# Optimization experiments

Hardware: AMD Instinct MI355X
Metric: run time of the kernel (lower is better)

Reference implementation:

```python
import jax, jax.numpy as jnp
import numpy as np

D_MODEL = 512
NHEAD = 8
HEAD_DIM = D_MODEL // NHEAD  # 64
BUCKETS = 32                 # lsh_hash_bucket_size; hashes >= 32 never attended (faithful to source loop)
N_HASHES = 2
B, T = 2, 2048


def setup_inputs() -> dict:
    key = jax.random.key(0)
    ks = jax.random.split(key, 14)
    s = 1.0 / np.sqrt(D_MODEL)
    sh = 1.0 / np.sqrt(HEAD_DIM)
    return {
        "query": jax.random.normal(ks[0], (B, T, D_MODEL), dtype=jnp.float32),
        "key": jax.random.normal(ks[1], (B, T, D_MODEL), dtype=jnp.float32),
        "value": jax.random.normal(ks[2], (B, T, D_MODEL), dtype=jnp.float32),
        "Wq": jax.random.normal(ks[3], (D_MODEL, D_MODEL), dtype=jnp.float32) * s,
        "bq": jnp.zeros((D_MODEL,), jnp.float32),
        "Wk": jax.random.normal(ks[4], (D_MODEL, D_MODEL), dtype=jnp.float32) * s,
        "bk": jnp.zeros((D_MODEL,), jnp.float32),
        "Wv": jax.random.normal(ks[5], (D_MODEL, D_MODEL), dtype=jnp.float32) * s,
        "bv": jnp.zeros((D_MODEL,), jnp.float32),
        "Wo": jax.random.normal(ks[6], (D_MODEL, D_MODEL), dtype=jnp.float32) * s,
        "bo": jnp.zeros((D_MODEL,), jnp.float32),
        "lsh_W": jax.random.normal(ks[7], (N_HASHES, HEAD_DIM, HEAD_DIM), dtype=jnp.float32) * sh,
        "lsh_b": jax.random.normal(ks[8], (N_HASHES, HEAD_DIM), dtype=jnp.float32) * sh,
    }


def reference(query, key, value, Wq, bq, Wk, bk, Wv, bv, Wo, bo, lsh_W, lsh_b):
    B0, Nt, E = query.shape
    H, Dh = NHEAD, E // NHEAD

    def lin(x, W, b):  # torch nn.Linear: x @ W.T + b
        return x @ W.T + b

    # Source transposes (0,1) then reshape(B0, Nt, H, Dh); reshape on the
    # contiguous transposed tensor == jnp reshape of swapaxes result.
    q = lin(jnp.swapaxes(query, 0, 1), Wq, bq).reshape(B0, Nt, H, Dh).transpose(0, 2, 1, 3)
    k = lin(jnp.swapaxes(key, 0, 1), Wk, bk).reshape(B0, Nt, H, Dh).transpose(0, 2, 1, 3)
    v = lin(jnp.swapaxes(value, 0, 1), Wv, bv).reshape(B0, Nt, H, Dh).transpose(0, 2, 1, 3)

    scale = 1.0 / jnp.sqrt(jnp.asarray(Dh, q.dtype))
    neg = jnp.finfo(q.dtype).min
    acc = jnp.zeros_like(q)
    for i in range(N_HASHES):
        # argmax(softmax(x)) == argmax(x)
        qh = jnp.argmax(q @ lsh_W[i].T + lsh_b[i], axis=-1)  # [B,H,T]
        kh = jnp.argmax(k @ lsh_W[i].T + lsh_b[i], axis=-1)  # [B,H,T]
        # attend only within same bucket AND bucket id < BUCKETS (source loops 0..BUCKETS-1)
        mask = (qh[..., :, None] == kh[..., None, :]) & (qh[..., :, None] < BUCKETS)
        scores = jnp.einsum('bhtd,bhsd->bhts', q, k) * scale
        probs = jax.nn.softmax(jnp.where(mask, scores, neg), axis=-1)
        valid = mask.any(axis=-1)  # queries with >=1 key in-bucket; others stay zero
        out_i = jnp.einsum('bhts,bhsd->bhtd', probs, v)
        acc = acc + jnp.where(valid[..., None], out_i, jnp.zeros((), q.dtype))
    out = acc / N_HASHES  # mean over hash rounds

    out = out.transpose(0, 2, 1, 3).reshape(B0, Nt, E)
    out = lin(out, Wo, bo)
    return jnp.swapaxes(out, 0, 1)  # [Nt, B0, E]
```

## Files before the change

kernel.cpp:

```cpp
#include <hip/hip_runtime.h>
#include <stdint.h>
#include <math.h>


#define T_ 2048
#define E_ 512
#define H_ 8
#define DH_ 64
#define B_ 2
#define M_ 4096
#define NROUND 2
#define NBUCKET 32
#define NSEG 32
#define MAXTASK 5120

typedef short v8s __attribute__((ext_vector_type(8)));
typedef _Float16 v8h __attribute__((ext_vector_type(8)));
typedef float v4f __attribute__((ext_vector_type(4)));

__device__ __forceinline__ float bf2f(uint16_t u) {
  union { uint32_t i; float f; } v; v.i = ((uint32_t)u) << 16; return v.f;
}
__device__ __forceinline__ uint16_t f2bf(float f) {
  union { float fv; uint32_t i; } v; v.fv = f;
  uint32_t x = v.i;
  x += 0x7fffu + ((x >> 16) & 1u);
  return (uint16_t)(x >> 16);
}
__device__ __forceinline__ void split8(const float4 a, const float4 b,
                                       v8s& h, v8s& l) {
  const float x[8] = {a.x, a.y, a.z, a.w, b.x, b.y, b.z, b.w};
#pragma unroll
  for (int j = 0; j < 8; j++) {
    const uint16_t hh = f2bf(x[j]);
    h[j] = (short)hh;
    l[j] = (short)f2bf(x[j] - bf2f(hh));
  }
}
__device__ __forceinline__ void split2h8(const float4 a, const float4 b,
                                         v8h& h, v8h& l) {
  const float x[8] = {a.x, a.y, a.z, a.w, b.x, b.y, b.z, b.w};
#pragma unroll
  for (int j = 0; j < 8; j++) {
    const float xv = x[j];
    const _Float16 hh = (fabsf(xv) < 6.1035156e-5f) ? (_Float16)0.0f
                                                    : (_Float16)xv;
    const float r = xv - (float)hh;
    h[j] = hh;
    l[j] = (_Float16)(r * 4096.0f);
  }
}

__global__ __launch_bounds__(256) void prep_kernel(
    const float* __restrict__ Xq, const float* __restrict__ Xk,
    const float* __restrict__ Xv,
    const float* __restrict__ Wq, const float* __restrict__ Wk,
    const float* __restrict__ Wv, const float* __restrict__ Wo,
    const float* __restrict__ lshW,
    uint16_t* __restrict__ Xqh, uint16_t* __restrict__ Xql,
    uint16_t* __restrict__ Xkh, uint16_t* __restrict__ Xkl,
    uint16_t* __restrict__ Xvh, uint16_t* __restrict__ Xvl,
    uint16_t* __restrict__ Wqh, uint16_t* __restrict__ Wql,
    uint16_t* __restrict__ Wkh, uint16_t* __restrict__ Wkl,
    uint16_t* __restrict__ Wvh, uint16_t* __restrict__ Wvl,
    uint16_t* __restrict__ Woh, uint16_t* __restrict__ Wol,
    uint16_t* __restrict__ Lwh, uint16_t* __restrict__ Lwl,
    float* __restrict__ attn, int* __restrict__ cnt)
{
  const int bid = blockIdx.x;
  const int tid = threadIdx.x;

  if (bid < 384) {
    const int sel = bid >> 7;
    const int mb  = bid & 127;
    const float* X = (sel == 0) ? Xq : (sel == 1) ? Xk : Xv;
    uint16_t* H = (sel == 0) ? Xqh : (sel == 1) ? Xkh : Xvh;
    uint16_t* L = (sel == 0) ? Xql : (sel == 1) ? Xkl : Xvl;
#pragma unroll
    for (int it = 0; it < 8; it++) {
      const int g = it * 256 + tid;
      const int f = g >> 6;
      const int lane = g & 63;
      const int ks = f >> 1, half = f & 1;
      const int p = mb * 32 + half * 16 + (lane & 15);
      const int k = ks * 32 + (lane >> 4) * 8;
      const long src = ((long)(p & 1) * T_ + (p >> 1)) * E_ + k;
      const float4 a = *(const float4*)(X + src);
      const float4 b = *(const float4*)(X + src + 4);
      v8h h, l;
      split2h8(a, b, h, l);
      const long dst = (long)mb * 16384 + (long)g * 8;
      *(v8h*)(H + dst) = h;
      *(v8h*)(L + dst) = l;
    }
    return;
  }

  if (bid < 896) {
    const int wsel = (bid - 384) >> 7;
    const int g2 = ((bid - 384) & 127) * 256 + tid;
    const int f = g2 >> 6;
    const int lane = g2 & 63;
    const int nb = f >> 4, ks = f & 15;
    const int n = nb * 16 + (lane & 15);
    const int k = ks * 32 + (lane >> 4) * 8;
    const long src = (long)n * E_ + k;
    const long dst = (long)g2 * 8;
    if (wsel < 3) {
      const float* S = (wsel == 0) ? Wq : (wsel == 1) ? Wk : Wv;
      const float4 a = *(const float4*)(S + src);
      const float4 b = *(const float4*)(S + src + 4);
      v8h h, l;
      split2h8(a, b, h, l);
      uint16_t* H = (wsel == 0) ? Wqh : (wsel == 1) ? Wkh : Wvh;
      uint16_t* L = (wsel == 0) ? Wql : (wsel == 1) ? Wkl : Wvl;
      *(v8h*)(H + dst) = h;
      *(v8h*)(L + dst) = l;
    } else {
      const float4 a = *(const float4*)(Wo + src);
      const float4 b = *(const float4*)(Wo + src + 4);
      v8s h, l;
      split8(a, b, h, l);
      *(v8s*)(Woh + dst) = h;
      *(v8s*)(Wol + dst) = l;
    }
    return;
  }

  if (bid < 1920) {
    float4* a4 = (float4*)attn;
    const int g = (bid - 896) * 512 + tid * 2;
    a4[g] = make_float4(0.f, 0.f, 0.f, 0.f);
    a4[g + 1] = make_float4(0.f, 0.f, 0.f, 0.f);
    return;
  }

  for (int i = tid; i < 2 * NSEG * NBUCKET + 1; i += 256) cnt[i] = 0;
  for (int i = tid; i < NROUND * DH_ * DH_; i += 256) {
    const float xv = lshW[i];
    const _Float16 hh = (fabsf(xv) < 6.1035156e-5f) ? (_Float16)0.0f
                                                    : (_Float16)xv;
    const float r = xv - (float)hh;
    *(_Float16*)(Lwh + i) = hh;
    *(_Float16*)(Lwl + i) = (_Float16)(r * 4096.0f);
  }
}

__global__ __launch_bounds__(256) void proj_mfma(
    const uint16_t* __restrict__ Aqh, const uint16_t* __restrict__ Aql,
    const uint16_t* __restrict__ Akh, const uint16_t* __restrict__ Akl,
    const uint16_t* __restrict__ Avh, const uint16_t* __restrict__ Avl,
    const uint16_t* __restrict__ Bqh, const uint16_t* __restrict__ Bql,
    const uint16_t* __restrict__ Bkh, const uint16_t* __restrict__ Bkl,
    const uint16_t* __restrict__ Bvh, const uint16_t* __restrict__ Bvl,
    const float* __restrict__ bq, const float* __restrict__ bk,
    const float* __restrict__ bv,
    float* __restrict__ Qo, float* __restrict__ Ko, float* __restrict__ Vo)
{
  const uint16_t *Ah, *Al, *Bh, *Bl;
  const float* bias; float* C;
  if (blockIdx.z == 0)      { Ah = Aqh; Al = Aql; Bh = Bqh; Bl = Bql; bias = bq; C = Qo; }
  else if (blockIdx.z == 1) { Ah = Akh; Al = Akl; Bh = Bkh; Bl = Bkl; bias = bk; C = Ko; }
  else                      { Ah = Avh; Al = Avl; Bh = Bvh; Bl = Bvl; bias = bv; C = Vo; }

  const int wid = threadIdx.x >> 6, lane = threadIdx.x & 63;
  const int mb = blockIdx.x * 4 + wid;
  const int nb0 = blockIdx.y * 4;
  const int m0 = mb * 32, n0 = blockIdx.y * 64;
  const int l15 = lane & 15, quad = lane >> 4;

  const long aB = (long)mb * 16384 + lane * 8;
  long bB[4];
#pragma unroll
  for (int j = 0; j < 4; j++) bB[j] = (long)(nb0 + j) * 8192 + lane * 8;

  v4f accH[2][4] = {};
  v4f accX[2][4] = {};

  v8h ah0 = *(const v8h*)(Ah + aB);
  v8h ah1 = *(const v8h*)(Ah + aB + 512);
  v8h al0 = *(const v8h*)(Al + aB);
  v8h al1 = *(const v8h*)(Al + aB + 512);
  v8h bh[4], bl[4];
#pragma unroll
  for (int j = 0; j < 4; j++) {
    bh[j] = *(const v8h*)(Bh + bB[j]);
    bl[j] = *(const v8h*)(Bl + bB[j]);
  }

  for (int ks = 0; ks < 16; ks++) {
    const int kn = (ks + 1) & 15;
    const v8h nah0 = *(const v8h*)(Ah + aB + kn * 1024);
    const v8h nah1 = *(const v8h*)(Ah + aB + kn * 1024 + 512);
    const v8h nal0 = *(const v8h*)(Al + aB + kn * 1024);
    const v8h nal1 = *(const v8h*)(Al + aB + kn * 1024 + 512);
    v8h nbh[4], nbl[4];
#pragma unroll
    for (int j = 0; j < 4; j++) {
      nbh[j] = *(const v8h*)(Bh + bB[j] + kn * 512);
      nbl[j] = *(const v8h*)(Bl + bB[j] + kn * 512);
    }

#pragma unroll
    for (int j = 0; j < 4; j++) {
      accH[0][j] = __builtin_amdgcn_mfma_f32_16x16x32_f16(ah0, bh[j], accH[0][j], 0, 0, 0);
      accH[1][j] = __builtin_amdgcn_mfma_f32_16x16x32_f16(ah1, bh[j], accH[1][j], 0, 0, 0);
    }
#pragma unroll
    for (int j = 0; j < 4; j++) {
      accX[0][j] = __builtin_amdgcn_mfma_f32_16x16x32_f16(ah0, bl[j], accX[0][j], 0, 0, 0);
      accX[1][j] = __builtin_amdgcn_mfma_f32_16x16x32_f16(ah1, bl[j], accX[1][j], 0, 0, 0);
    }
#pragma unroll
    for (int j = 0; j < 4; j++) {
      accX[0][j] = __builtin_amdgcn_mfma_f32_16x16x32_f16(al0, bh[j], accX[0][j], 0, 0, 0);
      accX[1][j] = __builtin_amdgcn_mfma_f32_16x16x32_f16(al1, bh[j], accX[1][j], 0, 0, 0);
    }

    ah0 = nah0; al0 = nal0; ah1 = nah1; al1 = nal1;
#pragma unroll
    for (int j = 0; j < 4; j++) { bh[j] = nbh[j]; bl[j] = nbl[j]; }
  }

#pragma unroll
  for (int i = 0; i < 2; i++)
#pragma unroll
    for (int j = 0; j < 4; j++) {
      const int colg = n0 + j * 16 + l15;
      const float bb = bias[colg];
#pragma unroll
      for (int r = 0; r < 4; r++) {
        const int mm = m0 + i * 16 + quad * 4 + r;
        C[(long)mm * E_ + colg] =
            accH[i][j][r] + accX[i][j][r] * (1.0f / 4096.0f) + bb;
      }
    }
}

__global__ __launch_bounds__(256) void mfma_gemm(
    const float* __restrict__ A,
    const uint16_t* __restrict__ Bht, const uint16_t* __restrict__ Blt,
    const float* __restrict__ bias, float* __restrict__ C)
{
  const int wid = threadIdx.x >> 6, lane = threadIdx.x & 63;
  const int mb = blockIdx.x * 4 + wid;
  const int m0 = mb * 32;
  const int nb0 = blockIdx.y * 4;
  const int n0 = blockIdx.y * 64;
  const int l15 = lane & 15, quad = lane >> 4;

  const long aB = (long)mb * 16384 + lane * 8;
  long bB[4];
#pragma unroll
  for (int j = 0; j < 4; j++) bB[j] = (long)(nb0 + j) * 8192 + lane * 8;

  v4f acc[2][4] = {};
  for (int ks = 0; ks < 16; ks++) {
    const long a0 = aB + ks * 1024;
    const long a1 = a0 + 512;
    v8s ah0, al0, ah1, al1;
    split8(*(const float4*)(A + a0), *(const float4*)(A + a0 + 4), ah0, al0);
    split8(*(const float4*)(A + a1), *(const float4*)(A + a1 + 4), ah1, al1);
    v8s bh[4], bl[4];
#pragma unroll
    for (int j = 0; j < 4; j++) {
      bh[j] = *(const v8s*)(Bht + bB[j] + ks * 512);
      bl[j] = *(const v8s*)(Blt + bB[j] + ks * 512);
    }
#pragma unroll
    for (int j = 0; j < 4; j++) {
      acc[0][j] = __builtin_amdgcn_mfma_f32_16x16x32_bf16(ah0, bh[j], acc[0][j], 0, 0, 0);
      acc[1][j] = __builtin_amdgcn_mfma_f32_16x16x32_bf16(ah1, bh[j], acc[1][j], 0, 0, 0);
    }
#pragma unroll
    for (int j = 0; j < 4; j++) {
      acc[0][j] = __builtin_amdgcn_mfma_f32_16x16x32_bf16(ah0, bl[j], acc[0][j], 0, 0, 0);
      acc[1][j] = __builtin_amdgcn_mfma_f32_16x16x32_bf16(ah1, bl[j], acc[1][j], 0, 0, 0);
    }
#pragma unroll
    for (int j = 0; j < 4; j++) {
      acc[0][j] = __builtin_amdgcn_mfma_f32_16x16x32_bf16(al0, bh[j], acc[0][j], 0, 0, 0);
      acc[1][j] = __builtin_amdgcn_mfma_f32_16x16x32_bf16(al1, bh[j], acc[1][j], 0, 0, 0);
    }
  }

#pragma unroll
  for (int i = 0; i < 2; i++)
#pragma unroll
    for (int j = 0; j < 4; j++) {
      const int colg = n0 + j * 16 + l15;
      const float bb = bias[colg];
#pragma unroll
      for (int r = 0; r < 4; r++) {
        const int mm = m0 + i * 16 + quad * 4 + r;
        const int crow = (mm & (T_ - 1)) * B_ + (mm >> 11);
        C[(long)crow * E_ + colg] = acc[i][j][r] + bb;
      }
    }
}

__global__ __launch_bounds__(256) void hash_mfma(
    const float* __restrict__ Q, const float* __restrict__ K,
    const uint16_t* __restrict__ Lwh, const uint16_t* __restrict__ Lwl,
    const float* __restrict__ lshb,
    int* __restrict__ qh, int* __restrict__ kh,
    int* __restrict__ qcnt, int* __restrict__ kcnt)
{
  const int comb = blockIdx.y;
  const int src = comb >> 1, r = comb & 1;
  const float* X = src ? K : Q;
  int* outh = src ? kh : qh;
  int* cnt  = src ? kcnt : qcnt;

  const int wid = threadIdx.x >> 6, lane = threadIdx.x & 63;
  const int m0 = (blockIdx.x * 4 + wid) * 32;
  const int l15 = lane & 15, quad = lane >> 4;

  v8h bh[4][2], bl[4][2];
#pragma unroll
  for (int n = 0; n < 4; n++)
#pragma unroll
    for (int k = 0; k < 2; k++) {
      const int o = r * (DH_ * DH_) + (n * 16 + l15) * DH_ + k * 32 + quad * 8;
      bh[n][k] = *(const v8h*)(Lwh + o);
      bl[n][k] = *(const v8h*)(Lwl + o);
    }

  v4f accH[2][4] = {};
  v4f accX[2][4] = {};
#pragma unroll
  for (int k = 0; k < 2; k++) {
    const long a0 = (long)(m0 + l15) * DH_ + k * 32 + quad * 8;
    const long a1 = a0 + 16L * DH_;
    v8h ah0, al0, ah1, al1;
    split2h8(*(const float4*)(X + a0), *(const float4*)(X + a0 + 4), ah0, al0);
    split2h8(*(const float4*)(X + a1), *(const float4*)(X + a1 + 4), ah1, al1);
#pragma unroll
    for (int n = 0; n < 4; n++) {
      accH[0][n] = __builtin_amdgcn_mfma_f32_16x16x32_f16(ah0, bh[n][k], accH[0][n], 0, 0, 0);
      accH[1][n] = __builtin_amdgcn_mfma_f32_16x16x32_f16(ah1, bh[n][k], accH[1][n], 0, 0, 0);
      accX[0][n] = __builtin_amdgcn_mfma_f32_16x16x32_f16(ah0, bl[n][k], accX[0][n], 0, 0, 0);
      accX[1][n] = __builtin_amdgcn_mfma_f32_16x16x32_f16(ah1, bl[n][k], accX[1][n], 0, 0, 0);
      accX[0][n] = __builtin_amdgcn_mfma_f32_16x16x32_f16(al0, bh[n][k], accX[0][n], 0, 0, 0);
      accX[1][n] = __builtin_amdgcn_mfma_f32_16x16x32_f16(al1, bh[n][k], accX[1][n], 0, 0, 0);
    }
  }

  float bb[4];
#pragma unroll
  for (int n = 0; n < 4; n++) bb[n] = lshb[r * DH_ + n * 16 + l15];

#pragma unroll
  for (int i = 0; i < 2; i++)
#pragma unroll
    for (int reg = 0; reg < 4; reg++) {
      float bv = -INFINITY; int bi = 0x7fffffff;
#pragma unroll
      for (int n = 0; n < 4; n++) {
        const float v = accH[i][n][reg] + accX[i][n][reg] * (1.0f / 4096.0f)
                        + bb[n];
        const int idx = n * 16 + l15;
        if (v > bv || (v == bv && idx < bi)) { bv = v; bi = idx; }
      }
#pragma unroll
      for (int d = 8; d >= 1; d >>= 1) {
        const float ov = __shfl_xor(bv, d);
        const int oi = __shfl_xor(bi, d);
        if (ov > bv || (ov == bv && oi < bi)) { bv = ov; bi = oi; }
      }
      if (l15 == 0) {
        const int hr = m0 + i * 16 + quad * 4 + reg;
        const int p = hr >> 3, hh = hr & 7;
        const int bt = p >> 11, t = p & (T_ - 1);
        const int seg = r * 16 + bt * H_ + hh;
        outh[seg * T_ + t] = bi;
        if (bi < NBUCKET) atomicAdd(&cnt[seg * NBUCKET + bi], 1);
      }
    }
}

__global__ __launch_bounds__(1024) void scan_kernel(
    const int* __restrict__ kcnt, int* __restrict__ koff,
    int* __restrict__ kcur,
    const int* __restrict__ qcnt, int* __restrict__ qoff,
    int* __restrict__ qcur,
    int* __restrict__ ntasks, int* __restrict__ tasks)
{
  const int tid = threadIdx.x;
  const int isq = blockIdx.x;
  const int seg = tid >> 5;
  const int b   = tid & 31;
  const int* cnt = isq ? qcnt : kcnt;
  int* off = isq ? qoff : koff;
  int* cur = isq ? qcur : kcur;

  const int c = cnt[seg * NBUCKET + b];

  int s = c;
#pragma unroll
  for (int d = 1; d < 32; d <<= 1) {
    const int t = __shfl_up(s, d, 32);
    if (b >= d) s += t;
  }
  const int excl = s - c;
  off[seg * (NBUCKET + 1) + b] = excl;
  cur[seg * NBUCKET + b] = excl;
  if (b == 31) off[seg * (NBUCKET + 1) + NBUCKET] = s;

  if (isq) {
    const int nt = (c + 15) >> 4;
    const int lane = tid & 63;
    int ws = nt;
#pragma unroll
    for (int d = 1; d < 64; d <<= 1) {
      const int t = __shfl_up(ws, d, 64);
      if (lane >= d) ws += t;
    }
    const int wtotal = __shfl(ws, 63, 64);
    int base = 0;
    if (lane == 63 && wtotal > 0) base = atomicAdd(ntasks, wtotal);
    base = __shfl(base, 63, 64);
    const int my = base + ws - nt;
    for (int i = 0; i < nt; i++)
      tasks[my + i] = (seg << 16) | (b << 8) | i;
  }
}

__global__ __launch_bounds__(256) void scatter2_kernel(
    const int* __restrict__ kh, const int* __restrict__ qh,
    int* __restrict__ kcur, int* __restrict__ qcur,
    int* __restrict__ klist, int* __restrict__ qlist)
{
  const int idx = blockIdx.x * 256 + threadIdx.x;
  const int y = blockIdx.y;
  const int* hsh = y ? qh : kh;
  int* cur = y ? qcur : kcur;
  int* list = y ? qlist : klist;
  const int v = hsh[idx];
  if (v < NBUCKET) {
    const int seg = idx >> 11;
    const int pos = atomicAdd(&cur[seg * NBUCKET + v], 1);
    list[seg * T_ + pos] = idx & (T_ - 1);
  }
}

__global__ __launch_bounds__(256) void attn_task(
    const float* __restrict__ Q, const float* __restrict__ K,
    const float* __restrict__ V,
    const int* __restrict__ qlist, const int* __restrict__ qoff,
    const int* __restrict__ klist, const int* __restrict__ koff,
    const int* __restrict__ tasks, const int* __restrict__ ntasks,
    float* __restrict__ attn)
{
  __shared__ __align__(16) float Plds[16][68];
  __shared__ __align__(16) float Vts[64][68];
  __shared__ float larr[16];

  if ((int)blockIdx.x >= *ntasks) return;
  const int tk = tasks[blockIdx.x];
  const int seg = tk >> 16, bucket = (tk >> 8) & 255, qt = tk & 255;
  const int ctx = seg & 15;
  const int b = ctx >> 3, h = ctx & 7;

  const int qlo = qoff[seg * (NBUCKET + 1) + bucket] + qt * 16;
  const int nqt = min(16, qoff[seg * (NBUCKET + 1) + bucket + 1] - qlo);
  const int klo = koff[seg * (NBUCKET + 1) + bucket];
  const int nk  = koff[seg * (NBUCKET + 1) + bucket + 1] - klo;
  if (nk == 0) return;

  const int tid = threadIdx.x;
  const int wid = tid >> 6, lane = tid & 63;
  const int l15 = lane & 15, quad = lane >> 4;
  const int r0 = tid >> 4, c4 = tid & 15;

  const float* Qb = Q + ((long)b * T_) * E_ + h * DH_;
  const float* Kb = K + ((long)b * T_) * E_ + h * DH_;
  const float* Vb = V + ((long)b * T_) * E_ + h * DH_;
  const int* ql = qlist + seg * T_;
  const int* kl = klist + seg * T_;

  if (tid < 16) larr[tid] = 0.f;

  const long qrow = (long)ql[qlo + min(l15, nqt - 1)] * E_;
  v8s qfh[2], qfl[2];
#pragma unroll
  for (int ks = 0; ks < 2; ks++) {
    const float4 a = *(const float4*)(Qb + qrow + ks * 32 + quad * 8);
    const float4 c = *(const float4*)(Qb + qrow + ks * 32 + quad * 8 + 4);
    split8(a, c, qfh[ks], qfl[ks]);
  }
  __syncthreads();

  v4f oacc = {0.f, 0.f, 0.f, 0.f};

  for (int kt = 0; kt < nk; kt += 64) {
    float4 vreg[4];
#pragma unroll
    for (int it = 0; it < 4; it++) {
      const int key = kt + it * 16 + r0;
      const long krow = (long)kl[klo + min(key, nk - 1)] * E_;
      vreg[it] = *(const float4*)(Vb + krow + c4 * 4);
    }

    const int keyg = kt + wid * 16 + l15;
    const long krow = (long)kl[klo + min(keyg, nk - 1)] * E_;
    v4f sacc = {0.f, 0.f, 0.f, 0.f};
#pragma unroll
    for (int ks = 0; ks < 2; ks++) {
      const float4 a = *(const float4*)(Kb + krow + ks * 32 + quad * 8);
      const float4 c = *(const float4*)(Kb + krow + ks * 32 + quad * 8 + 4);
      v8s kfh, kfl;
      split8(a, c, kfh, kfl);
      sacc = __builtin_amdgcn_mfma_f32_16x16x32_bf16(qfh[ks], kfh, sacc, 0, 0, 0);
      sacc = __builtin_amdgcn_mfma_f32_16x16x32_bf16(qfh[ks], kfl, sacc, 0, 0, 0);
      sacc = __builtin_amdgcn_mfma_f32_16x16x32_bf16(qfl[ks], kfh, sacc, 0, 0, 0);
    }

    const bool kvalid = keyg < nk;
    const float p0 = kvalid ? __expf(sacc[0] * 0.125f) : 0.f;
    const float p1 = kvalid ? __expf(sacc[1] * 0.125f) : 0.f;
    const float p2 = kvalid ? __expf(sacc[2] * 0.125f) : 0.f;
    const float p3 = kvalid ? __expf(sacc[3] * 0.125f) : 0.f;

    float rs0 = p0, rs1 = p1, rs2 = p2, rs3 = p3;
#pragma unroll
    for (int d = 1; d < 16; d <<= 1) {
      rs0 += __shfl_xor(rs0, d);
      rs1 += __shfl_xor(rs1, d);
      rs2 += __shfl_xor(rs2, d);
      rs3 += __shfl_xor(rs3, d);
    }
    if (l15 == 0) {
      atomicAdd(&larr[quad * 4 + 0], rs0);
      atomicAdd(&larr[quad * 4 + 1], rs1);
      atomicAdd(&larr[quad * 4 + 2], rs2);
      atomicAdd(&larr[quad * 4 + 3], rs3);
    }
    Plds[quad * 4 + 0][wid * 16 + l15] = p0;
    Plds[quad * 4 + 1][wid * 16 + l15] = p1;
    Plds[quad * 4 + 2][wid * 16 + l15] = p2;
    Plds[quad * 4 + 3][wid * 16 + l15] = p3;

#pragma unroll
    for (int it = 0; it < 4; it++) {
      const int row = it * 16 + r0;
      Vts[c4 * 4 + 0][row] = vreg[it].x;
      Vts[c4 * 4 + 1][row] = vreg[it].y;
      Vts[c4 * 4 + 2][row] = vreg[it].z;
      Vts[c4 * 4 + 3][row] = vreg[it].w;
    }
    __syncthreads();

#pragma unroll
    for (int ks = 0; ks < 2; ks++) {
      const float4 pa = *(const float4*)&Plds[l15][ks * 32 + quad * 8];
      const float4 pb = *(const float4*)&Plds[l15][ks * 32 + quad * 8 + 4];
      v8s pah, pal;
      split8(pa, pb, pah, pal);
      const float4 va = *(const float4*)&Vts[wid * 16 + l15][ks * 32 + quad * 8];
      const float4 vb = *(const float4*)&Vts[wid * 16 + l15][ks * 32 + quad * 8 + 4];
      v8s vfh, vfl;
      split8(va, vb, vfh, vfl);
      oacc = __builtin_amdgcn_mfma_f32_16x16x32_bf16(pah, vfh, oacc, 0, 0, 0);
      oacc = __builtin_amdgcn_mfma_f32_16x16x32_bf16(pah, vfl, oacc, 0, 0, 0);
      oacc = __builtin_amdgcn_mfma_f32_16x16x32_bf16(pal, vfh, oacc, 0, 0, 0);
    }
    __syncthreads();
  }

  const int kd = h * DH_ + wid * 16 + l15;
  const int kpart = (kd >> 5) * 2 * 512 + ((kd >> 3) & 3) * 16 * 8 + (kd & 7);
#pragma unroll
  for (int r = 0; r < 4; r++) {
    const int q = quad * 4 + r;
    if (q < nqt) {
      const float inv = 0.5f / larr[q];
      const int t = ql[qlo + q];
      const int p = b * T_ + t;
      const long off = (long)(p >> 5) * 16384 + ((p >> 4) & 1) * 512
                       + (p & 15) * 8 + kpart;
      atomicAdd(attn + off, oacc[r] * inv);
    }
  }
}

extern "C" void kernel_launch(void* const* d_in, const int* in_sizes, int n_in,
                              void* d_out, int out_size, void* d_ws, size_t ws_size,
                              hipStream_t stream) {
  const float* query = (const float*)d_in[0];
  const float* key   = (const float*)d_in[1];
  const float* value = (const float*)d_in[2];
  const float* Wq = (const float*)d_in[3];
  const float* bq = (const float*)d_in[4];
  const float* Wk = (const float*)d_in[5];
  const float* bk = (const float*)d_in[6];
  const float* Wv = (const float*)d_in[7];
  const float* bv = (const float*)d_in[8];
  const float* Wo = (const float*)d_in[9];
  const float* bo = (const float*)d_in[10];
  const float* lshW = (const float*)d_in[11];
  const float* lshb = (const float*)d_in[12];

  const size_t MSZ = (size_t)M_ * E_;
  const size_t WSZ = (size_t)E_ * E_;
  float* Q    = (float*)d_ws;
  float* K    = Q + MSZ;
  float* V    = K + MSZ;
  float* attn = V + MSZ;
  int* qh     = (int*)(attn + MSZ);
  int* kh     = qh + NSEG * T_;
  int* klist  = kh + NSEG * T_;
  int* qlist  = klist + NSEG * T_;
  int* kcnt   = qlist + NSEG * T_;
  int* qcnt   = kcnt + NSEG * NBUCKET;
  int* ntasks = qcnt + NSEG * NBUCKET;
  int* kcur   = ntasks + 1;
  int* qcur   = kcur + NSEG * NBUCKET;
  int* koff   = qcur + NSEG * NBUCKET;
  int* qoff   = koff + NSEG * (NBUCKET + 1);
  int* tasks  = qoff + NSEG * (NBUCKET + 1);
  uint16_t* Woh = (uint16_t*)(((uintptr_t)(tasks + MAXTASK) + 15) & ~(uintptr_t)15);
  uint16_t* Wol = Woh + WSZ;
  uint16_t* Wqh = Wol + WSZ;
  uint16_t* Wql = Wqh + WSZ;
  uint16_t* Wkh = Wql + WSZ;
  uint16_t* Wkl = Wkh + WSZ;
  uint16_t* Wvh = Wkl + WSZ;
  uint16_t* Wvl = Wvh + WSZ;
  uint16_t* Xqh = Wvl + WSZ;
  uint16_t* Xql = Xqh + MSZ;
  uint16_t* Xkh = Xql + MSZ;
  uint16_t* Xkl = Xkh + MSZ;
  uint16_t* Xvh = Xkl + MSZ;
  uint16_t* Xvl = Xvh + MSZ;
  uint16_t* Lwh = Xvl + MSZ;
  uint16_t* Lwl = Lwh + (size_t)NROUND * DH_ * DH_;

  prep_kernel<<<dim3(1921), 256, 0, stream>>>(
      query, key, value, Wq, Wk, Wv, Wo, lshW,
      Xqh, Xql, Xkh, Xkl, Xvh, Xvl,
      Wqh, Wql, Wkh, Wkl, Wvh, Wvl, Woh, Wol,
      Lwh, Lwl, attn, kcnt);
  proj_mfma<<<dim3(M_ / 128, E_ / 64, 3), 256, 0, stream>>>(
      Xqh, Xql, Xkh, Xkl, Xvh, Xvl,
      Wqh, Wql, Wkh, Wkl, Wvh, Wvl,
      bq, bk, bv, Q, K, V);
  hash_mfma<<<dim3(M_ * H_ / 128, 4), 256, 0, stream>>>(
      Q, K, Lwh, Lwl, lshb, qh, kh, qcnt, kcnt);
  scan_kernel<<<dim3(2), 1024, 0, stream>>>(kcnt, koff, kcur, qcnt, qoff, qcur,
                                            ntasks, tasks);
  scatter2_kernel<<<dim3(NSEG * T_ / 256, 2), 256, 0, stream>>>(
      kh, qh, kcur, qcur, klist, qlist);
  attn_task<<<dim3(MAXTASK), 256, 0, stream>>>(
      Q, K, V, qlist, qoff, klist, koff, tasks, ntasks, attn);
  mfma_gemm<<<dim3(M_ / 128, E_ / 64), 256, 0, stream>>>(
      attn, Woh, Wol, bo, (float*)d_out);
}
```

Before: 211.8 us.

## Process 32 queries per attention task to reuse K/V tiles

Each attention task now covers two 16-row query tiles instead of one, so every loaded K and V tile feeds twice as many MFMA operations and the number of tasks drops by roughly half. The goal is to cut redundant global loads of K/V rows and per-task overhead. In exchange each block does more serial work and uses more registers and LDS. There are fewer blocks to fill the GPU, and buckets with few queries waste half of the work.

```diff
diff --git a/kernel.cpp b/kernel.cpp
--- a/kernel.cpp
+++ b/kernel.cpp
@@ -408,7 +408,7 @@
   if (b == 31) off[seg * (NBUCKET + 1) + NBUCKET] = s;
 
   if (isq) {
-    const int nt = (c + 15) >> 4;
+    const int nt = (c + 31) >> 5;
     const int lane = tid & 63;
     int ws = nt;
 #pragma unroll
@@ -452,9 +452,9 @@
     const int* __restrict__ tasks, const int* __restrict__ ntasks,
     float* __restrict__ attn)
 {
-  __shared__ __align__(16) float Plds[16][68];
+  __shared__ __align__(16) float Plds[32][68];
   __shared__ __align__(16) float Vts[64][68];
-  __shared__ float larr[16];
+  __shared__ float larr[32];
 
   if ((int)blockIdx.x >= *ntasks) return;
   const int tk = tasks[blockIdx.x];
@@ -462,8 +462,8 @@
   const int ctx = seg & 15;
   const int b = ctx >> 3, h = ctx & 7;
 
-  const int qlo = qoff[seg * (NBUCKET + 1) + bucket] + qt * 16;
-  const int nqt = min(16, qoff[seg * (NBUCKET + 1) + bucket + 1] - qlo);
+  const int qlo = qoff[seg * (NBUCKET + 1) + bucket] + qt * 32;
+  const int nqt = min(32, qoff[seg * (NBUCKET + 1) + bucket + 1] - qlo);
   const int klo = koff[seg * (NBUCKET + 1) + bucket];
   const int nk  = koff[seg * (NBUCKET + 1) + bucket + 1] - klo;
   if (nk == 0) return;
@@ -479,19 +479,22 @@
   const int* ql = qlist + seg * T_;
   const int* kl = klist + seg * T_;
 
-  if (tid < 16) larr[tid] = 0.f;
-
-  const long qrow = (long)ql[qlo + min(l15, nqt - 1)] * E_;
-  v8s qfh[2], qfl[2];
-#pragma unroll
-  for (int ks = 0; ks < 2; ks++) {
-    const float4 a = *(const float4*)(Qb + qrow + ks * 32 + quad * 8);
-    const float4 c = *(const float4*)(Qb + qrow + ks * 32 + quad * 8 + 4);
-    split8(a, c, qfh[ks], qfl[ks]);
+  if (tid < 32) larr[tid] = 0.f;
+
+  v8s qfh[2][2], qfl[2][2];
+#pragma unroll
+  for (int i = 0; i < 2; i++) {
+    const long qrow = (long)ql[qlo + min(i * 16 + l15, nqt - 1)] * E_;
+#pragma unroll
+    for (int ks = 0; ks < 2; ks++) {
+      const float4 a = *(const float4*)(Qb + qrow + ks * 32 + quad * 8);
+      const float4 c = *(const float4*)(Qb + qrow + ks * 32 + quad * 8 + 4);
+      split8(a, c, qfh[i][ks], qfl[i][ks]);
+    }
   }
   __syncthreads();
 
-  v4f oacc = {0.f, 0.f, 0.f, 0.f};
+  v4f oacc[2] = {{0.f, 0.f, 0.f, 0.f}, {0.f, 0.f, 0.f, 0.f}};
 
   for (int kt = 0; kt < nk; kt += 64) {
     float4 vreg[4];
@@ -504,42 +507,48 @@
 
     const int keyg = kt + wid * 16 + l15;
     const long krow = (long)kl[klo + min(keyg, nk - 1)] * E_;
-    v4f sacc = {0.f, 0.f, 0.f, 0.f};
+    v4f sacc[2] = {{0.f, 0.f, 0.f, 0.f}, {0.f, 0.f, 0.f, 0.f}};
 #pragma unroll
     for (int ks = 0; ks < 2; ks++) {
       const float4 a = *(const float4*)(Kb + krow + ks * 32 + quad * 8);
       const float4 c = *(const float4*)(Kb + krow + ks * 32 + quad * 8 + 4);
       v8s kfh, kfl;
       split8(a, c, kfh, kfl);
-      sacc = __builtin_amdgcn_mfma_f32_16x16x32_bf16(qfh[ks], kfh, sacc, 0, 0, 0);
-      sacc = __builtin_amdgcn_mfma_f32_16x16x32_bf16(qfh[ks], kfl, sacc, 0, 0, 0);
-      sacc = __builtin_amdgcn_mfma_f32_16x16x32_bf16(qfl[ks], kfh, sacc, 0, 0, 0);
+#pragma unroll
+      for (int i = 0; i < 2; i++) {
+        sacc[i] = __builtin_amdgcn_mfma_f32_16x16x32_bf16(qfh[i][ks], kfh, sacc[i], 0, 0, 0);
+        sacc[i] = __builtin_amdgcn_mfma_f32_16x16x32_bf16(qfh[i][ks], kfl, sacc[i], 0, 0, 0);
+        sacc[i] = __builtin_amdgcn_mfma_f32_16x16x32_bf16(qfl[i][ks], kfh, sacc[i], 0, 0, 0);
+      }
     }
 
     const bool kvalid = keyg < nk;
-    const float p0 = kvalid ? __expf(sacc[0] * 0.125f) : 0.f;
-    const float p1 = kvalid ? __expf(sacc[1] * 0.125f) : 0.f;
-    const float p2 = kvalid ? __expf(sacc[2] * 0.125f) : 0.f;
-    const float p3 = kvalid ? __expf(sacc[3] * 0.125f) : 0.f;
-
-    float rs0 = p0, rs1 = p1, rs2 = p2, rs3 = p3;
-#pragma unroll
-    for (int d = 1; d < 16; d <<= 1) {
-      rs0 += __shfl_xor(rs0, d);
-      rs1 += __shfl_xor(rs1, d);
-      rs2 += __shfl_xor(rs2, d);
-      rs3 += __shfl_xor(rs3, d);
-    }
-    if (l15 == 0) {
-      atomicAdd(&larr[quad * 4 + 0], rs0);
-      atomicAdd(&larr[quad * 4 + 1], rs1);
-      atomicAdd(&larr[quad * 4 + 2], rs2);
-      atomicAdd(&larr[quad * 4 + 3], rs3);
-    }
-    Plds[quad * 4 + 0][wid * 16 + l15] = p0;
-    Plds[quad * 4 + 1][wid * 16 + l15] = p1;
-    Plds[quad * 4 + 2][wid * 16 + l15] = p2;
-    Plds[quad * 4 + 3][wid * 16 + l15] = p3;
+#pragma unroll
+    for (int i = 0; i < 2; i++) {
+      const float p0 = kvalid ? __expf(sacc[i][0] * 0.125f) : 0.f;
+      const float p1 = kvalid ? __expf(sacc[i][1] * 0.125f) : 0.f;
+      const float p2 = kvalid ? __expf(sacc[i][2] * 0.125f) : 0.f;
+      const float p3 = kvalid ? __expf(sacc[i][3] * 0.125f) : 0.f;
+
+      float rs0 = p0, rs1 = p1, rs2 = p2, rs3 = p3;
+#pragma unroll
+      for (int d = 1; d < 16; d <<= 1) {
+        rs0 += __shfl_xor(rs0, d);
+        rs1 += __shfl_xor(rs1, d);
+        rs2 += __shfl_xor(rs2, d);
+        rs3 += __shfl_xor(rs3, d);
+      }
+      if (l15 == 0) {
+        atomicAdd(&larr[i * 16 + quad * 4 + 0], rs0);
+        atomicAdd(&larr[i * 16 + quad * 4 + 1], rs1);
+        atomicAdd(&larr[i * 16 + quad * 4 + 2], rs2);
+        atomicAdd(&larr[i * 16 + quad * 4 + 3], rs3);
+      }
+      Plds[i * 16 + quad * 4 + 0][wid * 16 + l15] = p0;
+      Plds[i * 16 + quad * 4 + 1][wid * 16 + l15] = p1;
+      Plds[i * 16 + quad * 4 + 2][wid * 16 + l15] = p2;
+      Plds[i * 16 + quad * 4 + 3][wid * 16 + l15] = p3;
+    }
 
 #pragma unroll
     for (int it = 0; it < 4; it++) {
@@ -553,17 +562,20 @@
 
 #pragma unroll
     for (int ks = 0; ks < 2; ks++) {
-      const float4 pa = *(const float4*)&Plds[l15][ks * 32 + quad * 8];
-      const float4 pb = *(const float4*)&Plds[l15][ks * 32 + quad * 8 + 4];
-      v8s pah, pal;
-      split8(pa, pb, pah, pal);
       const float4 va = *(const float4*)&Vts[wid * 16 + l15][ks * 32 + quad * 8];
       const float4 vb = *(const float4*)&Vts[wid * 16 + l15][ks * 32 + quad * 8 + 4];
       v8s vfh, vfl;
       split8(va, vb, vfh, vfl);
-      oacc = __builtin_amdgcn_mfma_f32_16x16x32_bf16(pah, vfh, oacc, 0, 0, 0);
-      oacc = __builtin_amdgcn_mfma_f32_16x16x32_bf16(pah, vfl, oacc, 0, 0, 0);
-      oacc = __builtin_amdgcn_mfma_f32_16x16x32_bf16(pal, vfh, oacc, 0, 0, 0);
+#pragma unroll
+      for (int i = 0; i < 2; i++) {
+        const float4 pa = *(const float4*)&Plds[i * 16 + l15][ks * 32 + quad * 8];
+        const float4 pb = *(const float4*)&Plds[i * 16 + l15][ks * 32 + quad * 8 + 4];
+        v8s pah, pal;
+        split8(pa, pb, pah, pal);
+        oacc[i] = __builtin_amdgcn_mfma_f32_16x16x32_bf16(pah, vfh, oacc[i], 0, 0, 0);
+        oacc[i] = __builtin_amdgcn_mfma_f32_16x16x32_bf16(pah, vfl, oacc[i], 0, 0, 0);
+        oacc[i] = __builtin_amdgcn_mfma_f32_16x16x32_bf16(pal, vfh, oacc[i], 0, 0, 0);
+      }
     }
     __syncthreads();
   }
@@ -571,17 +583,19 @@
   const int kd = h * DH_ + wid * 16 + l15;
   const int kpart = (kd >> 5) * 2 * 512 + ((kd >> 3) & 3) * 16 * 8 + (kd & 7);
 #pragma unroll
-  for (int r = 0; r < 4; r++) {
-    const int q = quad * 4 + r;
-    if (q < nqt) {
-      const float inv = 0.5f / larr[q];
-      const int t = ql[qlo + q];
-      const int p = b * T_ + t;
-      const long off = (long)(p >> 5) * 16384 + ((p >> 4) & 1) * 512
-                       + (p & 15) * 8 + kpart;
-      atomicAdd(attn + off, oacc[r] * inv);
-    }
-  }
+  for (int i = 0; i < 2; i++)
+#pragma unroll
+    for (int r = 0; r < 4; r++) {
+      const int q = i * 16 + quad * 4 + r;
+      if (q < nqt) {
+        const float inv = 0.5f / larr[q];
+        const int t = ql[qlo + q];
+        const int p = b * T_ + t;
+        const long off = (long)(p >> 5) * 16384 + ((p >> 4) & 1) * 512
+                         + (p & 15) * 8 + kpart;
+        atomicAdd(attn + off, oacc[i][r] * inv);
+      }
+    }
 }
 
 extern "C" void kernel_launch(void* const* d_in, const int* in_sizes, int n_in,
```

New measurement: 217.1 us. 2.5% more time.
